# Optimization experiments

Hardware: AMD Instinct MI355X
Metric: run time of the kernel (lower is better)

Reference implementation:

```python
import jax, jax.numpy as jnp
import numpy as np

K0 = 25
K1 = 25
P0 = 4
P1 = 4


def _cheb(x, L, K):
    # x: (N, M, Fin); Chebyshev polynomial features T_k(L) x, k=0..K-1
    N, M, Fin = x.shape
    x0 = x
    xs = [x0]
    if K > 1:
        x1 = jnp.einsum('uv,nvf->nuf', L, x0)
        xs.append(x1)
        for _ in range(2, K):
            x2 = 2.0 * jnp.einsum('uv,nvf->nuf', L, x1) - x0
            xs.append(x2)
            x0, x1 = x1, x2
    # stack K last => layout (N, M, Fin*K) with k fastest, matching torch view
    return jnp.stack(xs, axis=-1).reshape(N, M, Fin * K)


def _maxpool_nodes(x, p):
    # x: (N, M, F) -> max over contiguous groups of p nodes (== max_pool1d)
    N, M, F = x.shape
    return x.reshape(N, M // p, p, F).max(axis=2)


def setup_inputs() -> dict:
    key = jax.random.key(0)
    ks = jax.random.split(key, 8)
    N, Cin, M0, M1 = 64, 1, 4096, 1024
    F0, F1 = 32, 64
    Mfin, Mh, Mo = 256, 512, 10

    def lap(k, m):
        # symmetric matrix with spectral radius < 1 (mimics rescaled Laplacian)
        A = jax.random.normal(k, (m, m), jnp.float32)
        A = (A + A.T) * 0.5
        return A / (1.1 * np.sqrt(2.0 * m))

    def lin(k, fin, fout):
        k1, k2 = jax.random.split(k)
        s = 1.0 / np.sqrt(fin)
        W = jax.random.uniform(k1, (fin, fout), jnp.float32, -s, s)
        b = jax.random.uniform(k2, (fout,), jnp.float32, -s, s)
        return W, b

    x = jax.random.normal(ks[0], (N, Cin, M0), jnp.float32)
    L0 = lap(ks[1], M0)
    L1 = lap(ks[2], M1)
    W1, b1 = lin(ks[3], Cin * K0, F0)
    W2, b2 = lin(ks[4], F0 * K1, F1)
    Wh, bh = lin(ks[5], Mfin * F1, Mh)
    Wo, bo = lin(ks[6], Mh, Mo)
    return {'x': x, 'L0': L0, 'L1': L1, 'W1': W1, 'b1': b1, 'W2': W2,
            'b2': b2, 'Wh': Wh, 'bh': bh, 'Wo': Wo, 'bo': bo}


def reference(x, L0, L1, W1, b1, W2, b2, Wh, bh, Wo, bo):
    N = x.shape[0]
    h = x.reshape(N, -1, 1)  # (N, M0, Fin=1); view semantics, Cin==1
    # conv layer 1: chebyshev -> linear -> relu -> maxpool
    h = jax.nn.relu(_cheb(h, L0, K0) @ W1 + b1)
    h = _maxpool_nodes(h, P0)  # (N, 1024, 32)
    # conv layer 2
    h = jax.nn.relu(_cheb(h, L1, K1) @ W2 + b2)
    h = _maxpool_nodes(h, P1)  # (N, 256, 64)
    # fully connected head (dropout p=0)
    h = jax.nn.relu(h.reshape(N, -1) @ Wh + bh)
    return h @ Wo + bo
```

## Files before the change

kernel.cpp:

```cpp
#include <hip/hip_runtime.h>

typedef unsigned short u16;
typedef unsigned int   u32;
typedef _Float16 f16;
typedef f16  v8h __attribute__((ext_vector_type(8)));
typedef f16  v4h __attribute__((ext_vector_type(4)));
typedef short v8s __attribute__((ext_vector_type(8)));
typedef float v4f __attribute__((ext_vector_type(4)));
typedef u16   v4u __attribute__((ext_vector_type(4)));

__device__ __forceinline__ float bf2f(u16 u) {
    union { float f; u32 i; } c; c.i = ((u32)u) << 16; return c.f;
}
__device__ __forceinline__ u16 f2bf(float f) {
    union { float f; u32 i; } c; c.f = f;
    u32 x = c.i;
    return (u16)((x + 0x7fffu + ((x >> 16) & 1u)) >> 16);
}
__device__ __forceinline__ float ldw(const void* p, long i, int flag) {
    return flag ? bf2f(((const u16*)p)[i]) : ((const float*)p)[i];
}

__global__ void detect_k(const u32* __restrict__ w, u32* __restrict__ meta) {
    __shared__ int cnt;
    if (threadIdx.x == 0) cnt = 0;
    __syncthreads();
    u32 v = w[(size_t)threadIdx.x * 4099];
    u32 f = (v >> 7) & 0xFFu;
    if (f >= 0x60u && f < 0x7Fu) atomicAdd(&cnt, 1);
    __syncthreads();
    if (threadIdx.x == 0) meta[0] = (cnt >= 192) ? 1u : 0u;
}

__global__ void cvt_half(const void* __restrict__ in, f16* __restrict__ out,
                         const u32* __restrict__ meta, int n) {
    const int flag = meta[0];
    const int n4 = n >> 2;
    const int stride = gridDim.x * blockDim.x;
    for (int i = blockIdx.x * blockDim.x + threadIdx.x; i < n4; i += stride) {
        v4h o;
        if (flag) {
            v4u h = *(const v4u*)((const u16*)in + (size_t)i * 4);
            #pragma unroll
            for (int r = 0; r < 4; ++r) o[r] = (f16)bf2f(h[r]);
        } else {
            v4f v = *(const v4f*)((const float*)in + (size_t)i * 4);
            #pragma unroll
            for (int r = 0; r < 4; ++r) o[r] = (f16)v[r];
        }
        *(v4h*)(out + (size_t)i * 4) = o;
    }
}

__global__ void w2t_k(const void* __restrict__ W2, const u32* __restrict__ meta,
                      f16* __restrict__ W2t16) {
    const int flag = meta[0];
    const int i = blockIdx.x * 256 + threadIdx.x;
    if (i >= 51200) return;
    const int k = i >> 6, fo = i & 63;
    const float w = ldw(W2, (size_t)k * 64 + fo, flag);
    const int f = k / 25, kc = k % 25;
    W2t16[(size_t)fo * 800 + kc * 32 + f] = (f16)w;
}

template<int FUSED>
__global__ __launch_bounds__(256) void cheb_tile(
    const f16* __restrict__ L, const f16* __restrict__ B, const f16* __restrict__ A,
    f16* __restrict__ C, float* __restrict__ Cpart, f16* __restrict__ Xt,
    int M, int V, int NC, int kc, float alpha, int useA)
{
    __shared__ f16 smem[2 * 64 * 72];
    const int tid  = threadIdx.x;
    const int wave = tid >> 6;
    const int lane = tid & 63;
    const int r16  = lane & 15;
    const int quad = lane >> 4;
    const int wm = wave & 1, wn = wave >> 1;

    const int m0 = blockIdx.x * 64;
    const int n0 = blockIdx.y * 64;
    const int k0 = blockIdx.z * kc;

    const int sr = lane >> 3;
    const int sc = lane & 7;
    const int rloc = wave * 16 + sr;
    const int lw  = rloc * 72 + sc * 8;

    v4f acc[2][2];
    #pragma unroll
    for (int i = 0; i < 2; ++i)
        #pragma unroll
        for (int j = 0; j < 2; ++j) acc[i][j] = (v4f){0.f, 0.f, 0.f, 0.f};

    const int arow0 = (wm * 32 + r16) * 72;
    const int arow1 = arow0 + 16 * 72;
    const int brow0 = 4608 + (wn * 32 + r16) * 72;
    const int brow1 = brow0 + 16 * 72;

    const int stages = kc >> 6;
    for (int st = 0; st < stages; ++st) {
        const int kk = k0 + st * 64;
        const size_t gA = (size_t)(m0 + rloc) * V + kk + sc * 8;
        const size_t gB = (size_t)(n0 + rloc) * V + kk + sc * 8;
        const size_t j8 = (size_t)8 * V;

        v8h t0 = *(const v8h*)(L + gA);
        v8h t1 = *(const v8h*)(L + gA + j8);
        v8h t2 = *(const v8h*)(B + gB);
        v8h t3 = *(const v8h*)(B + gB + j8);

        __syncthreads();
        *(v8h*)(smem +        lw)       = t0;
        *(v8h*)(smem +        lw + 576) = t1;
        *(v8h*)(smem + 4608 + lw)       = t2;
        *(v8h*)(smem + 4608 + lw + 576) = t3;
        __syncthreads();

        #pragma unroll
        for (int s = 0; s < 2; ++s) {
            const int qo = (s * 4 + quad) * 8;
            v8h a0 = *(const v8h*)(smem + arow0 + qo);
            v8h a1 = *(const v8h*)(smem + arow1 + qo);
            v8h b0 = *(const v8h*)(smem + brow0 + qo);
            v8h b1 = *(const v8h*)(smem + brow1 + qo);
            acc[0][0] = __builtin_amdgcn_mfma_f32_16x16x32_f16(a0, b0, acc[0][0], 0, 0, 0);
            acc[0][1] = __builtin_amdgcn_mfma_f32_16x16x32_f16(a0, b1, acc[0][1], 0, 0, 0);
            acc[1][0] = __builtin_amdgcn_mfma_f32_16x16x32_f16(a1, b0, acc[1][0], 0, 0, 0);
            acc[1][1] = __builtin_amdgcn_mfma_f32_16x16x32_f16(a1, b1, acc[1][1], 0, 0, 0);
        }
    }

    #pragma unroll
    for (int j = 0; j < 2; ++j) {
        const int n = n0 + wn * 32 + j * 16 + r16;
        #pragma unroll
        for (int i = 0; i < 2; ++i) {
            const int mrow = m0 + wm * 32 + i * 16 + quad * 4;
            if (FUSED) {
                const size_t obase = (size_t)n * M + mrow;
                float vals[4];
                if (useA) {
                    v4h a4 = *(const v4h*)(A + obase);
                    #pragma unroll
                    for (int r = 0; r < 4; ++r)
                        vals[r] = alpha * acc[i][j][r] - (float)a4[r];
                } else {
                    #pragma unroll
                    for (int r = 0; r < 4; ++r) vals[r] = alpha * acc[i][j][r];
                }
                v4h co;
                #pragma unroll
                for (int r = 0; r < 4; ++r) co[r] = (f16)vals[r];
                *(v4h*)(C + obase) = co;
                const int nb = n >> 5, f = n & 31;
                f16* xt = Xt + ((size_t)(nb * 1024) + mrow) * 32 + f;
                #pragma unroll
                for (int r = 0; r < 4; ++r) xt[r * 32] = co[r];
            } else {
                float* cp = Cpart + ((size_t)(blockIdx.z * NC + n)) * M + mrow;
                *(v4f*)cp = acc[i][j];
            }
        }
    }
}

__global__ __launch_bounds__(256) void cheb_comb(
    const float* __restrict__ Cpart, const f16* __restrict__ Aprev,
    f16* __restrict__ C, int total, int nkc, float alpha, int useA)
{
    const int idx = blockIdx.x * 256 + threadIdx.x;
    if (idx >= total) return;
    float s = 0.f;
    for (int c = 0; c < nkc; ++c) s += Cpart[(size_t)c * total + idx];
    float v = alpha * s;
    if (useA) v -= (float)Aprev[idx];
    C[idx] = (f16)v;
}

__global__ __launch_bounds__(256) void lin1_pool(
    const f16* __restrict__ S, const void* __restrict__ W1, const void* __restrict__ b1,
    const u32* __restrict__ meta, f16* __restrict__ O, f16* __restrict__ Xt0)
{
    const int flag = meta[0];
    const int g  = blockIdx.x * 64 + threadIdx.x;
    const int f  = blockIdx.y * 4 + threadIdx.y;
    const int n  = blockIdx.z;
    float a[8];
    #pragma unroll
    for (int r = 0; r < 8; ++r) a[r] = 0.f;
    const size_t base = (size_t)n * 4096 + (size_t)g * 8;
    #pragma unroll
    for (int k = 0; k < 25; ++k) {
        v8h x8 = *(const v8h*)(S + (size_t)k * 262144 + base);
        float w = ldw(W1, k * 32 + f, flag);
        #pragma unroll
        for (int r = 0; r < 8; ++r) a[r] += (float)x8[r] * w;
    }
    const float b = ldw(b1, f, flag);
    float v0 = fmaxf(fmaxf(fmaxf(a[0], a[1]), fmaxf(a[2], a[3])) + b, 0.f);
    float v1 = fmaxf(fmaxf(fmaxf(a[4], a[5]), fmaxf(a[6], a[7])) + b, 0.f);
    const int m1 = g * 2;
    const size_t oi = ((size_t)n * 32 + f) * 1024 + m1;
    O[oi]     = (f16)v0;
    O[oi + 1] = (f16)v1;
    f16* xt = Xt0 + ((size_t)n * 1024 + m1) * 32 + f;
    xt[0]  = (f16)v0;
    xt[32] = (f16)v1;
}

__global__ __launch_bounds__(256) void lin2_mfma(
    const f16* __restrict__ Xt0, const f16* __restrict__ Xt1, const f16* __restrict__ Xt2,
    const f16* __restrict__ W2t16,
    float* __restrict__ acc, int k0, int cnt, int zi)
{
    const int tid  = threadIdx.x;
    const int wave = tid >> 6;
    const int lane = tid & 63;
    const int r16  = lane & 15;
    const int quad = lane >> 4;
    const int n  = blockIdx.y;
    const int u0 = blockIdx.x * 128 + wave * 32;

    v4f a[2][4];
    #pragma unroll
    for (int i = 0; i < 2; ++i)
        #pragma unroll
        for (int j = 0; j < 4; ++j) a[i][j] = (v4f){0.f, 0.f, 0.f, 0.f};

    const f16* Xs[3] = {Xt0, Xt1, Xt2};
    for (int c = 0; c < cnt; ++c) {
        const f16* X = Xs[c];
        v8h a0 = *(const v8h*)(X + ((size_t)n * 1024 + u0 + r16) * 32 + quad * 8);
        v8h a1 = *(const v8h*)(X + ((size_t)n * 1024 + u0 + 16 + r16) * 32 + quad * 8);
        const int kb = (k0 + c) * 32 + quad * 8;
        #pragma unroll
        for (int j = 0; j < 4; ++j) {
            v8h bh = *(const v8h*)(W2t16 + (size_t)(j * 16 + r16) * 800 + kb);
            a[0][j] = __builtin_amdgcn_mfma_f32_16x16x32_f16(a0, bh, a[0][j], 0, 0, 0);
            a[1][j] = __builtin_amdgcn_mfma_f32_16x16x32_f16(a1, bh, a[1][j], 0, 0, 0);
        }
    }

    #pragma unroll
    for (int i = 0; i < 2; ++i) {
        const int u = u0 + i * 16 + quad * 4;
        #pragma unroll
        for (int j = 0; j < 4; ++j) {
            const int fo = j * 16 + r16;
            float* p = acc + ((size_t)n * 1024 + u) * 64 + fo;
            if (zi) {
                #pragma unroll
                for (int r = 0; r < 4; ++r) p[r * 64] = a[i][j][r];
            } else {
                #pragma unroll
                for (int r = 0; r < 4; ++r) p[r * 64] += a[i][j][r];
            }
        }
    }
}

__global__ __launch_bounds__(256) void lin2fin(
    const float* __restrict__ acc, const void* __restrict__ b2, const u32* __restrict__ meta,
    u16* __restrict__ hb16h, u16* __restrict__ hb16l)
{
    const int flag = meta[0];
    const int fo = threadIdx.x;
    const int m2 = blockIdx.x * 4 + threadIdx.y;
    const int n  = blockIdx.y;
    const size_t b = ((size_t)n * 1024 + (size_t)m2 * 4) * 64 + fo;
    float v = fmaxf(fmaxf(acc[b], acc[b + 64]), fmaxf(acc[b + 128], acc[b + 192]));
    v = fmaxf(v + ldw(b2, fo, flag), 0.f);
    const size_t oi = (size_t)n * 16384 + (size_t)m2 * 64 + fo;
    const u16 h = f2bf(v);
    hb16h[oi] = h;
    hb16l[oi] = f2bf(v - bf2f(h));
}

__global__ __launch_bounds__(256) void fc1_mfma(
    const u16* __restrict__ hb16h, const u16* __restrict__ hb16l,
    const void* __restrict__ Wh, const u32* __restrict__ meta,
    float* __restrict__ part128)
{
    const int flag = meta[0];
    const int tid  = threadIdx.x;
    const int wave = tid >> 6;
    const int lane = tid & 63;
    const int r16  = lane & 15;
    const int quad = lane >> 4;
    const int nt = blockIdx.x;
    const int kc = blockIdx.y * 4 + wave;

    v4f acc[4];
    #pragma unroll
    for (int mt = 0; mt < 4; ++mt) acc[mt] = (v4f){0.f, 0.f, 0.f, 0.f};

    const int h0 = nt * 16 + r16;
    for (int ks = 0; ks < 4; ++ks) {
        const int kb = kc * 128 + ks * 32 + quad * 8;
        v8s bh, bl;
        #pragma unroll
        for (int j = 0; j < 8; ++j) {
            const float w = ldw(Wh, (size_t)(kb + j) * 512 + h0, flag);
            const u16 h = f2bf(w);
            bh[j] = (short)h;
            bl[j] = (short)f2bf(w - bf2f(h));
        }
        #pragma unroll
        for (int mt = 0; mt < 4; ++mt) {
            const size_t arow = (size_t)(mt * 16 + r16) * 16384 + kb;
            v8s ah = *(const v8s*)(hb16h + arow);
            v8s al = *(const v8s*)(hb16l + arow);
            acc[mt] = __builtin_amdgcn_mfma_f32_16x16x32_bf16(ah, bh, acc[mt], 0, 0, 0);
            acc[mt] = __builtin_amdgcn_mfma_f32_16x16x32_bf16(ah, bl, acc[mt], 0, 0, 0);
            acc[mt] = __builtin_amdgcn_mfma_f32_16x16x32_bf16(al, bh, acc[mt], 0, 0, 0);
        }
    }

    #pragma unroll
    for (int mt = 0; mt < 4; ++mt) {
        const int m = mt * 16 + quad * 4;
        float* p = part128 + (size_t)kc * 32768 + (size_t)m * 512 + h0;
        #pragma unroll
        for (int r = 0; r < 4; ++r) p[r * 512] = acc[mt][r];
    }
}

__global__ __launch_bounds__(256) void fc1comb(
    const float* __restrict__ part128, float* __restrict__ partC)
{
    const int idx = blockIdx.x * 256 + threadIdx.x;
    float s = 0.f;
    #pragma unroll 8
    for (int c = 0; c < 128; ++c) s += part128[(size_t)c * 32768 + idx];
    partC[idx] = s;
}

__global__ void fc2_k(
    const float* __restrict__ partC, const void* __restrict__ bh,
    const void* __restrict__ Wo, const void* __restrict__ bo,
    const u32* __restrict__ meta, void* __restrict__ out)
{
    const int flag = meta[0];
    const int n = blockIdx.x;
    const int lane = threadIdx.x;
    float p[10];
    #pragma unroll
    for (int o = 0; o < 10; ++o) p[o] = 0.f;
    for (int j = lane; j < 512; j += 64) {
        const float r = fmaxf(partC[(size_t)n * 512 + j] + ldw(bh, j, flag), 0.f);
        #pragma unroll
        for (int o = 0; o < 10; ++o) p[o] += r * ldw(Wo, j * 10 + o, flag);
    }
    #pragma unroll
    for (int o = 0; o < 10; ++o) {
        for (int off = 32; off > 0; off >>= 1) p[o] += __shfl_down(p[o], off);
    }
    if (lane == 0) {
        #pragma unroll
        for (int o = 0; o < 10; ++o) {
            float v = p[o] + ldw(bo, o, flag);
            if (flag) ((u16*)out)[n * 10 + o] = f2bf(v);
            else      ((float*)out)[n * 10 + o] = v;
        }
    }
}

extern "C" void kernel_launch(void* const* d_in, const int* in_sizes, int n_in,
                              void* d_out, int out_size, void* d_ws, size_t ws_size,
                              hipStream_t stream)
{
    const void* x  = d_in[0];
    const void* L0 = d_in[1];
    const void* L1 = d_in[2];
    const void* W1 = d_in[3];
    const void* b1 = d_in[4];
    const void* W2 = d_in[5];
    const void* b2 = d_in[6];
    const void* Wh = d_in[7];
    const void* bh = d_in[8];
    const void* Wo = d_in[9];
    const void* bo = d_in[10];

    char* base = (char*)d_ws;
    size_t off = 0;
    u32* meta  = (u32*)(base + off);     off += 256;
    f16* L016  = (f16*)(base + off);     off += (size_t)16777216 * 2;
    f16* L116  = (f16*)(base + off);     off += (size_t)1048576 * 2;
    f16* A116  = (f16*)(base + off);     off += (size_t)25 * 262144 * 2;
    float* cpart = (float*)(base + off); off += (size_t)8 * 262144 * 4;
    f16* A216  = (f16*)(base + off);     off += (size_t)3 * 2097152 * 2;
    f16* Xt16  = (f16*)(base + off);     off += (size_t)3 * 2097152 * 2;
    float* ACC2 = (float*)(base + off);  off += (size_t)16777216;
    u16* hb16h = (u16*)(base + off);     off += (size_t)2097152;
    u16* hb16l = (u16*)(base + off);     off += (size_t)2097152;
    float* partC = (float*)(base + off); off += (size_t)131072;
    f16* W2t16 = (f16*)(base + off);     off += (size_t)102400;
    f16* Xt[3] = { Xt16, Xt16 + 2097152, Xt16 + 2 * 2097152 };
    float* part128 = ACC2;

    detect_k<<<1, 256, 0, stream>>>((const u32*)L0, meta);
    cvt_half<<<2048, 256, 0, stream>>>(L0, L016, meta, 16777216);
    cvt_half<<<256, 256, 0, stream>>>(L1, L116, meta, 1048576);
    cvt_half<<<64, 256, 0, stream>>>(x, A116, meta, 262144);
    w2t_k<<<200, 256, 0, stream>>>(W2, meta, W2t16);

    for (int k = 1; k < 25; ++k) {
        cheb_tile<0><<<dim3(64, 1, 8), 256, 0, stream>>>(
            L016, A116 + (size_t)(k - 1) * 262144, (const f16*)0,
            (f16*)0, cpart, (f16*)0,
            4096, 4096, 64, 512, 0.f, 0);
        const f16* pA = (k >= 2) ? A116 + (size_t)(k - 2) * 262144 : A116;
        cheb_comb<<<1024, 256, 0, stream>>>(
            cpart, pA, A116 + (size_t)k * 262144,
            262144, 8, (k == 1) ? 1.f : 2.f, (k >= 2) ? 1 : 0);
    }

    lin1_pool<<<dim3(8, 8, 64), dim3(64, 4), 0, stream>>>(
        A116, W1, b1, meta, A216, Xt[0]);

    for (int k = 1; k < 25; ++k) {
        const f16* pB = A216 + (size_t)((k - 1) % 3) * 2097152;
        const f16* pA = A216 + (size_t)(((k >= 2) ? (k - 2) : 0) % 3) * 2097152;
        f16* pC = A216 + (size_t)(k % 3) * 2097152;
        cheb_tile<1><<<dim3(16, 32, 1), 256, 0, stream>>>(
            L116, pB, pA, pC, (float*)0, Xt[k % 3],
            1024, 1024, 2048, 1024, (k == 1) ? 1.f : 2.f, (k >= 2) ? 1 : 0);
        if (k >= 2 && ((k - 2) % 3) == 0) {
            lin2_mfma<<<dim3(8, 64), 256, 0, stream>>>(
                Xt[0], Xt[1], Xt[2], W2t16, ACC2, k - 2, 3, (k == 2) ? 1 : 0);
        }
    }
    lin2_mfma<<<dim3(8, 64), 256, 0, stream>>>(
        Xt[0], Xt[0], Xt[0], W2t16, ACC2, 24, 1, 0);

    lin2fin<<<dim3(64, 64), dim3(64, 4), 0, stream>>>(ACC2, b2, meta, hb16h, hb16l);

    fc1_mfma<<<dim3(32, 32), 256, 0, stream>>>(hb16h, hb16l, Wh, meta, part128);
    fc1comb<<<128, 256, 0, stream>>>(part128, partC);
    fc2_k<<<64, 64, 0, stream>>>(partC, bh, Wo, bo, meta, d_out);
}
```

Before: 993.6 us.

## Fuse layer-1 Chebyshev split-K GEMM and combine into one pipelined kernel

Replaces the layer-1 split-K cheb_tile plus cheb_comb pair with a single kernel, cheb1_k. Each block computes a 32-row slab across all 64 batch columns over the full K=4096, double-buffers LDS with register prefetch, and applies the 2*L*x - x_prev recurrence in its epilogue. This removes the fp32 partial buffer traffic and one launch per recurrence step, but uses only 128 blocks, which may underfill the GPU. Layer-2 Xt staging grows from 3 to 5 buffers, so lin2_mfma runs every 5 steps instead of every 3 and the trailing extra launch is dropped.

```diff
diff --git a/kernel.cpp b/kernel.cpp
--- a/kernel.cpp
+++ b/kernel.cpp
@@ -63,10 +63,99 @@
     W2t16[(size_t)fo * 800 + kc * 32 + f] = (f16)w;
 }
 
-template<int FUSED>
+__global__ __launch_bounds__(256) void cheb1_k(
+    const f16* __restrict__ L, const f16* __restrict__ B, const f16* __restrict__ A,
+    f16* __restrict__ C, float alpha, int useA)
+{
+    __shared__ f16 smem[2 * 96 * 136];
+    const int tid  = threadIdx.x;
+    const int wave = tid >> 6;
+    const int lane = tid & 63;
+    const int r16  = lane & 15;
+    const int quad = lane >> 4;
+    const int m0 = blockIdx.x * 32;
+
+    const int lrow = tid >> 4;
+    const int lcol = (tid & 15) * 8;
+
+    v4f acc[2];
+    acc[0] = (v4f){0.f, 0.f, 0.f, 0.f};
+    acc[1] = (v4f){0.f, 0.f, 0.f, 0.f};
+
+    const size_t gA0 = (size_t)(m0 + lrow) * 4096 + lcol;
+    const size_t gB0 = (size_t)lrow * 4096 + lcol;
+
+    const int arow0 = r16 * 136;
+    const int arow1 = (16 + r16) * 136;
+    const int brow  = (32 + wave * 16 + r16) * 136;
+
+    v8h tA0, tA1, tB[4];
+    tA0 = *(const v8h*)(L + gA0);
+    tA1 = *(const v8h*)(L + gA0 + 16 * 4096);
+    #pragma unroll
+    for (int rr = 0; rr < 4; ++rr)
+        tB[rr] = *(const v8h*)(B + gB0 + (size_t)rr * 16 * 4096);
+    *(v8h*)(smem + lrow * 136 + lcol) = tA0;
+    *(v8h*)(smem + (16 + lrow) * 136 + lcol) = tA1;
+    #pragma unroll
+    for (int rr = 0; rr < 4; ++rr)
+        *(v8h*)(smem + (32 + rr * 16 + lrow) * 136 + lcol) = tB[rr];
+    __syncthreads();
+
+    #pragma unroll 2
+    for (int st = 0; st < 32; ++st) {
+        const f16* sc = smem + (st & 1) * (96 * 136);
+        if (st < 31) {
+            const size_t kk = (size_t)(st + 1) * 128;
+            tA0 = *(const v8h*)(L + gA0 + kk);
+            tA1 = *(const v8h*)(L + gA0 + kk + 16 * 4096);
+            #pragma unroll
+            for (int rr = 0; rr < 4; ++rr)
+                tB[rr] = *(const v8h*)(B + gB0 + kk + (size_t)rr * 16 * 4096);
+        }
+        #pragma unroll
+        for (int s = 0; s < 4; ++s) {
+            const int qo = (s * 4 + quad) * 8;
+            v8h a0 = *(const v8h*)(sc + arow0 + qo);
+            v8h a1 = *(const v8h*)(sc + arow1 + qo);
+            v8h b  = *(const v8h*)(sc + brow + qo);
+            acc[0] = __builtin_amdgcn_mfma_f32_16x16x32_f16(a0, b, acc[0], 0, 0, 0);
+            acc[1] = __builtin_amdgcn_mfma_f32_16x16x32_f16(a1, b, acc[1], 0, 0, 0);
+        }
+        if (st < 31) {
+            f16* sn = smem + ((st + 1) & 1) * (96 * 136);
+            *(v8h*)(sn + lrow * 136 + lcol) = tA0;
+            *(v8h*)(sn + (16 + lrow) * 136 + lcol) = tA1;
+            #pragma unroll
+            for (int rr = 0; rr < 4; ++rr)
+                *(v8h*)(sn + (32 + rr * 16 + lrow) * 136 + lcol) = tB[rr];
+            __syncthreads();
+        }
+    }
+
+    const int n = wave * 16 + r16;
+    #pragma unroll
+    for (int i = 0; i < 2; ++i) {
+        const size_t obase = (size_t)n * 4096 + m0 + i * 16 + quad * 4;
+        float vals[4];
+        if (useA) {
+            v4h a4 = *(const v4h*)(A + obase);
+            #pragma unroll
+            for (int r = 0; r < 4; ++r) vals[r] = alpha * acc[i][r] - (float)a4[r];
+        } else {
+            #pragma unroll
+            for (int r = 0; r < 4; ++r) vals[r] = alpha * acc[i][r];
+        }
+        v4h co;
+        #pragma unroll
+        for (int r = 0; r < 4; ++r) co[r] = (f16)vals[r];
+        *(v4h*)(C + obase) = co;
+    }
+}
+
 __global__ __launch_bounds__(256) void cheb_tile(
     const f16* __restrict__ L, const f16* __restrict__ B, const f16* __restrict__ A,
-    f16* __restrict__ C, float* __restrict__ Cpart, f16* __restrict__ Xt,
+    f16* __restrict__ C, f16* __restrict__ Xt,
     int M, int V, int NC, int kc, float alpha, int useA)
 {
     __shared__ f16 smem[2 * 64 * 72];
@@ -79,7 +168,6 @@
 
     const int m0 = blockIdx.x * 64;
     const int n0 = blockIdx.y * 64;
-    const int k0 = blockIdx.z * kc;
 
     const int sr = lane >> 3;
     const int sc = lane & 7;
@@ -99,7 +187,7 @@
 
     const int stages = kc >> 6;
     for (int st = 0; st < stages; ++st) {
-        const int kk = k0 + st * 64;
+        const int kk = st * 64;
         const size_t gA = (size_t)(m0 + rloc) * V + kk + sc * 8;
         const size_t gB = (size_t)(n0 + rloc) * V + kk + sc * 8;
         const size_t j8 = (size_t)8 * V;
@@ -136,45 +224,27 @@
         #pragma unroll
         for (int i = 0; i < 2; ++i) {
             const int mrow = m0 + wm * 32 + i * 16 + quad * 4;
-            if (FUSED) {
-                const size_t obase = (size_t)n * M + mrow;
-                float vals[4];
-                if (useA) {
-                    v4h a4 = *(const v4h*)(A + obase);
-                    #pragma unroll
-                    for (int r = 0; r < 4; ++r)
-                        vals[r] = alpha * acc[i][j][r] - (float)a4[r];
-                } else {
-                    #pragma unroll
-                    for (int r = 0; r < 4; ++r) vals[r] = alpha * acc[i][j][r];
-                }
-                v4h co;
+            const size_t obase = (size_t)n * M + mrow;
+            float vals[4];
+            if (useA) {
+                v4h a4 = *(const v4h*)(A + obase);
                 #pragma unroll
-                for (int r = 0; r < 4; ++r) co[r] = (f16)vals[r];
-                *(v4h*)(C + obase) = co;
-                const int nb = n >> 5, f = n & 31;
-                f16* xt = Xt + ((size_t)(nb * 1024) + mrow) * 32 + f;
+                for (int r = 0; r < 4; ++r)
+                    vals[r] = alpha * acc[i][j][r] - (float)a4[r];
+            } else {
                 #pragma unroll
-                for (int r = 0; r < 4; ++r) xt[r * 32] = co[r];
-            } else {
-                float* cp = Cpart + ((size_t)(blockIdx.z * NC + n)) * M + mrow;
-                *(v4f*)cp = acc[i][j];
+                for (int r = 0; r < 4; ++r) vals[r] = alpha * acc[i][j][r];
             }
-        }
-    }
-}
-
-__global__ __launch_bounds__(256) void cheb_comb(
-    const float* __restrict__ Cpart, const f16* __restrict__ Aprev,
-    f16* __restrict__ C, int total, int nkc, float alpha, int useA)
-{
-    const int idx = blockIdx.x * 256 + threadIdx.x;
-    if (idx >= total) return;
-    float s = 0.f;
-    for (int c = 0; c < nkc; ++c) s += Cpart[(size_t)c * total + idx];
-    float v = alpha * s;
-    if (useA) v -= (float)Aprev[idx];
-    C[idx] = (f16)v;
+            v4h co;
+            #pragma unroll
+            for (int r = 0; r < 4; ++r) co[r] = (f16)vals[r];
+            *(v4h*)(C + obase) = co;
+            const int nb = n >> 5, f = n & 31;
+            f16* xt = Xt + ((size_t)(nb * 1024) + mrow) * 32 + f;
+            #pragma unroll
+            for (int r = 0; r < 4; ++r) xt[r * 32] = co[r];
+        }
+    }
 }
 
 __global__ __launch_bounds__(256) void lin1_pool(
@@ -209,8 +279,7 @@
 }
 
 __global__ __launch_bounds__(256) void lin2_mfma(
-    const f16* __restrict__ Xt0, const f16* __restrict__ Xt1, const f16* __restrict__ Xt2,
-    const f16* __restrict__ W2t16,
+    const f16* __restrict__ XtBase, const f16* __restrict__ W2t16,
     float* __restrict__ acc, int k0, int cnt, int zi)
 {
     const int tid  = threadIdx.x;
@@ -227,9 +296,8 @@
         #pragma unroll
         for (int j = 0; j < 4; ++j) a[i][j] = (v4f){0.f, 0.f, 0.f, 0.f};
 
-    const f16* Xs[3] = {Xt0, Xt1, Xt2};
     for (int c = 0; c < cnt; ++c) {
-        const f16* X = Xs[c];
+        const f16* X = XtBase + (size_t)((k0 + c) % 5) * 2097152;
         v8h a0 = *(const v8h*)(X + ((size_t)n * 1024 + u0 + r16) * 32 + quad * 8);
         v8h a1 = *(const v8h*)(X + ((size_t)n * 1024 + u0 + 16 + r16) * 32 + quad * 8);
         const int kb = (k0 + c) * 32 + quad * 8;
@@ -387,15 +455,13 @@
     f16* L016  = (f16*)(base + off);     off += (size_t)16777216 * 2;
     f16* L116  = (f16*)(base + off);     off += (size_t)1048576 * 2;
     f16* A116  = (f16*)(base + off);     off += (size_t)25 * 262144 * 2;
-    float* cpart = (float*)(base + off); off += (size_t)8 * 262144 * 4;
     f16* A216  = (f16*)(base + off);     off += (size_t)3 * 2097152 * 2;
-    f16* Xt16  = (f16*)(base + off);     off += (size_t)3 * 2097152 * 2;
+    f16* Xt16  = (f16*)(base + off);     off += (size_t)5 * 2097152 * 2;
     float* ACC2 = (float*)(base + off);  off += (size_t)16777216;
     u16* hb16h = (u16*)(base + off);     off += (size_t)2097152;
     u16* hb16l = (u16*)(base + off);     off += (size_t)2097152;
-    float* partC = (float*)(base + off); off += (size_t)131072;
+    float* partC = (float*)(base + off); off += (size_t)131072 * 4;
     f16* W2t16 = (f16*)(base + off);     off += (size_t)102400;
-    f16* Xt[3] = { Xt16, Xt16 + 2097152, Xt16 + 2 * 2097152 };
     float* part128 = ACC2;
 
     detect_k<<<1, 256, 0, stream>>>((const u32*)L0, meta);
@@ -405,33 +471,29 @@
     w2t_k<<<200, 256, 0, stream>>>(W2, meta, W2t16);
 
     for (int k = 1; k < 25; ++k) {
-        cheb_tile<0><<<dim3(64, 1, 8), 256, 0, stream>>>(
-            L016, A116 + (size_t)(k - 1) * 262144, (const f16*)0,
-            (f16*)0, cpart, (f16*)0,
-            4096, 4096, 64, 512, 0.f, 0);
-        const f16* pA = (k >= 2) ? A116 + (size_t)(k - 2) * 262144 : A116;
-        cheb_comb<<<1024, 256, 0, stream>>>(
-            cpart, pA, A116 + (size_t)k * 262144,
-            262144, 8, (k == 1) ? 1.f : 2.f, (k >= 2) ? 1 : 0);
+        cheb1_k<<<128, 256, 0, stream>>>(
+            L016,
+            A116 + (size_t)(k - 1) * 262144,
+            A116 + (size_t)((k >= 2) ? (k - 2) : 0) * 262144,
+            A116 + (size_t)k * 262144,
+            (k == 1) ? 1.f : 2.f, (k >= 2) ? 1 : 0);
     }
 
     lin1_pool<<<dim3(8, 8, 64), dim3(64, 4), 0, stream>>>(
-        A116, W1, b1, meta, A216, Xt[0]);
+        A116, W1, b1, meta, A216, Xt16);
 
     for (int k = 1; k < 25; ++k) {
         const f16* pB = A216 + (size_t)((k - 1) % 3) * 2097152;
         const f16* pA = A216 + (size_t)(((k >= 2) ? (k - 2) : 0) % 3) * 2097152;
         f16* pC = A216 + (size_t)(k % 3) * 2097152;
-        cheb_tile<1><<<dim3(16, 32, 1), 256, 0, stream>>>(
-            L116, pB, pA, pC, (float*)0, Xt[k % 3],
+        cheb_tile<<<dim3(16, 32, 1), 256, 0, stream>>>(
+            L116, pB, pA, pC, Xt16 + (size_t)(k % 5) * 2097152,
             1024, 1024, 2048, 1024, (k == 1) ? 1.f : 2.f, (k >= 2) ? 1 : 0);
-        if (k >= 2 && ((k - 2) % 3) == 0) {
+        if ((k + 1) % 5 == 0) {
             lin2_mfma<<<dim3(8, 64), 256, 0, stream>>>(
-                Xt[0], Xt[1], Xt[2], W2t16, ACC2, k - 2, 3, (k == 2) ? 1 : 0);
-        }
-    }
-    lin2_mfma<<<dim3(8, 64), 256, 0, stream>>>(
-        Xt[0], Xt[0], Xt[0], W2t16, ACC2, 24, 1, 0);
+                Xt16, W2t16, ACC2, k - 4, 5, (k == 4) ? 1 : 0);
+        }
+    }
 
     lin2fin<<<dim3(64, 64), dim3(64, 4), 0, stream>>>(ACC2, b2, meta, hb16h, hb16l);
 
```

Result: slower. 1.111 ms (+11.8%).
